# Optimization experiments

Measured on AMD Instinct MI355X. Metric: run time of the kernel, lower is better.

The kernel has to match this reference:

```python
import jax, jax.numpy as jnp
import numpy as np

S = 60            # voxel grid side
N = 100000        # active voxels
M_PAD = 60000     # padded pairs per kernel offset
C_IN = 64
C_OUT = 64
KV = 27           # kernel volume (3^3)
CENTER = 13


def _build_maps():
    rng = np.random.default_rng(0)
    lin = rng.choice(S ** 3, size=N, replace=False)
    coords = np.stack(np.unravel_index(lin, (S, S, S)), axis=1).astype(np.int64)  # [N,3]
    lut = -np.ones(S ** 3, dtype=np.int64)
    lut[lin] = np.arange(N)
    imap = -np.ones((KV - 1, M_PAD), dtype=np.int32)
    omap = -np.ones((KV - 1, M_PAD), dtype=np.int32)
    row = 0
    for k in range(KV):
        if k == CENTER:
            continue
        d = np.array([k // 9 - 1, (k // 3) % 3 - 1, k % 3 - 1])
        nb = coords + d
        valid = np.all((nb >= 0) & (nb < S), axis=1)
        linnb = nb[:, 0] * S * S + nb[:, 1] * S + nb[:, 2]
        j = np.where(valid, lut[np.clip(linnb, 0, S ** 3 - 1)], -1)
        mask = j >= 0
        src = np.nonzero(mask)[0].astype(np.int32)   # input idx (gather)
        dst = j[mask].astype(np.int32)               # output idx (scatter)
        m = min(src.shape[0], M_PAD)
        imap[row, :m] = src[:m]
        omap[row, :m] = dst[:m]
        row += 1
    return imap, omap


def setup_inputs() -> dict:
    key = jax.random.key(0)
    kf, kw = jax.random.split(key)
    feats = jax.random.normal(kf, (N, C_IN), dtype=jnp.float32)
    stdv = 1.0 / np.sqrt(C_OUT * KV)
    kernel = jax.random.uniform(kw, (KV, C_IN, C_OUT), dtype=jnp.float32,
                                minval=-stdv, maxval=stdv)
    imap_np, omap_np = _build_maps()
    return {
        "feats": feats,
        "kernel": kernel,
        "imap": jnp.asarray(imap_np),
        "omap": jnp.asarray(omap_np),
    }


def reference(feats, kernel, imap, omap):
    # Submanifold sparse 3D conv: center weight applied densely,
    # 26 neighbor offsets via gather -> per-offset GEMM -> scatter-add.
    # feats: [N, Cin], kernel: [27, Cin, Cout], imap/omap: [26, M] (-1 = pad)
    koff = jnp.concatenate([jnp.arange(CENTER), jnp.arange(CENTER + 1, KV)])
    w_off = kernel[koff]                                   # [26, Cin, Cout]
    out = feats @ kernel[CENTER]                           # [N, Cout] center GEMM
    valid = (imap >= 0)                                    # [26, M]
    gathered = feats[jnp.clip(imap, 0)] * valid[..., None].astype(feats.dtype)  # [26, M, Cin]
    partial = jnp.einsum('kmc,kco->kmo', gathered, w_off)  # [26, M, Cout]
    dst = jnp.where(valid, omap, 0).reshape(-1)            # padded rows contribute zeros
    out = out.at[dst].add(partial.reshape(-1, partial.shape[-1]))
    return out
```

## Files before the change

kernel.cpp:

```cpp
#include <hip/hip_runtime.h>


#define N_PTS 100000
#define MPAD  60000
#define C     64
#define NSL   27

typedef short bf16x8 __attribute__((ext_vector_type(8)));
typedef float f32x4  __attribute__((ext_vector_type(4)));

static __device__ inline unsigned short f2bf(float x) {
    unsigned int u = __float_as_uint(x);
    u += 0x7fffu + ((u >> 16) & 1u);
    return (unsigned short)(u >> 16);
}

#define FEATS16_BYTES ((size_t)(N_PTS + 1) * C * 2)
#define WFRAG_OFF     (((FEATS16_BYTES) + 255) & ~(size_t)255)
#define WFRAG_BYTES   ((size_t)NSL * 2 * 4 * 64 * 16)
#define NBR_OFF       (WFRAG_OFF + WFRAG_BYTES)
#define NBR_BYTES     ((size_t)26 * N_PTS * 4)

#define FEAT_ITEMS 800008
#define WF_ITEMS   (NSL * 2 * 4 * 64)
#define NBRF_ITEMS (26 * N_PTS / 4)
#define PREP_TOTAL (FEAT_ITEMS + WF_ITEMS + NBRF_ITEMS)

__global__ __launch_bounds__(256) void prep_all(const float* __restrict__ feats,
                                                const float* __restrict__ kern,
                                                unsigned short* __restrict__ f16,
                                                unsigned short* __restrict__ wf,
                                                int* __restrict__ nbr) {
    const int idx = blockIdx.x * 256 + threadIdx.x;
    if (idx < FEAT_ITEMS) {
        bf16x8* dst = (bf16x8*)f16;
        if (idx < FEAT_ITEMS - 8) {
            const float4* src = (const float4*)feats;
            const float4 a = src[2 * idx];
            const float4 b = src[2 * idx + 1];
            bf16x8 v;
            v[0] = (short)f2bf(a.x); v[1] = (short)f2bf(a.y);
            v[2] = (short)f2bf(a.z); v[3] = (short)f2bf(a.w);
            v[4] = (short)f2bf(b.x); v[5] = (short)f2bf(b.y);
            v[6] = (short)f2bf(b.z); v[7] = (short)f2bf(b.w);
            dst[idx] = v;
        } else {
            dst[idx] = (bf16x8){0, 0, 0, 0, 0, 0, 0, 0};
        }
    } else if (idx < FEAT_ITEMS + WF_ITEMS) {
        const int w = idx - FEAT_ITEMS;
        const int lane = w & 63;
        const int rest = w >> 6;
        const int ct = rest & 3;
        const int kk = (rest >> 2) & 1;
        const int s  = rest >> 3;
        const int q = lane >> 4, t = lane & 15;
        const int ksrc = (s == 26) ? 13 : (s + (s >= 13 ? 1 : 0));
        const int k0 = kk * 32 + q * 8;
        const int n  = ct * 16 + t;
        const float* wp = kern + (size_t)ksrc * 4096 + n;
        bf16x8 v;
        #pragma unroll
        for (int j = 0; j < 8; ++j) v[j] = (short)f2bf(wp[(size_t)(k0 + j) * 64]);
        ((bf16x8*)wf)[w] = v;
    } else {
        const int k = idx - (FEAT_ITEMS + WF_ITEMS);
        if (k < NBRF_ITEMS) ((int4*)nbr)[k] = make_int4(-1, -1, -1, -1);
    }
}

__global__ __launch_bounds__(256) void prep_nbr(const int* __restrict__ imap,
                                                const int* __restrict__ omap,
                                                int* __restrict__ nbr) {
    const int v = blockIdx.x * 256 + threadIdx.x;
    const int s = blockIdx.y;
    if (v >= MPAD / 4) return;
    const int4 iv = ((const int4*)(imap + (size_t)s * MPAD))[v];
    const int4 ov = ((const int4*)(omap + (size_t)s * MPAD))[v];
    int* nb = nbr + (size_t)s * N_PTS;
    if (iv.x >= 0) nb[ov.x] = iv.x;
    if (iv.y >= 0) nb[ov.y] = iv.y;
    if (iv.z >= 0) nb[ov.z] = iv.z;
    if (iv.w >= 0) nb[ov.w] = iv.w;
}

__global__ __launch_bounds__(256) void spconv_main(const unsigned short* __restrict__ f16,
                                                   const unsigned short* __restrict__ wf,
                                                   const int* __restrict__ nbr,
                                                   float* __restrict__ out) {
    const int lane = threadIdx.x & 63;
    const int wave = threadIdx.x >> 6;
    const int q = lane >> 4, t = lane & 15;
    const int R0 = blockIdx.x * 128 + wave * 32;
    const int row0 = R0 + t;
    const int row1 = R0 + 16 + t;

    const bf16x8* wfv = (const bf16x8*)wf;
    const bf16x8* fv  = (const bf16x8*)f16;

    auto ldj = [&](int s, int row) -> int {
        if (s == 26) return (row < N_PTS) ? row : -1;
        const int rc = (row < N_PTS) ? row : 0;
        const int j = nbr[(size_t)s * N_PTS + rc];
        return (row < N_PTS) ? j : -1;
    };
    auto clampj = [&](int j) -> int {
        return ((unsigned)j < (unsigned)N_PTS) ? j : N_PTS;
    };

    f32x4 acc[2][4];
    #pragma unroll
    for (int a = 0; a < 2; ++a)
        #pragma unroll
        for (int c = 0; c < 4; ++c)
            acc[a][c] = (f32x4){0.f, 0.f, 0.f, 0.f};

    int j0[NSL], j1[NSL];
    bf16x8 A[NSL][4];

    j0[0] = ldj(0, row0); j1[0] = ldj(0, row1);
    j0[1] = ldj(1, row0); j1[1] = ldj(1, row1);
    {
        const bf16x8* a0 = fv + (size_t)clampj(j0[0]) * 8;
        const bf16x8* a1 = fv + (size_t)clampj(j1[0]) * 8;
        A[0][0] = a0[q]; A[0][1] = a0[4 + q];
        A[0][2] = a1[q]; A[0][3] = a1[4 + q];
    }

    #pragma unroll
    for (int s = 0; s < NSL; ++s) {
        if (s + 2 < NSL) {
            j0[s + 2] = ldj(s + 2, row0);
            j1[s + 2] = ldj(s + 2, row1);
        }
        if (s + 1 < NSL) {
            const bf16x8* a0 = fv + (size_t)clampj(j0[s + 1]) * 8;
            const bf16x8* a1 = fv + (size_t)clampj(j1[s + 1]) * 8;
            A[s + 1][0] = a0[q]; A[s + 1][1] = a0[4 + q];
            A[s + 1][2] = a1[q]; A[s + 1][3] = a1[4 + q];
        }
        bf16x8 B0[4], B1[4];
        #pragma unroll
        for (int ct = 0; ct < 4; ++ct) {
            B0[ct] = wfv[s * 512 + ct * 64 + lane];
            B1[ct] = wfv[s * 512 + 256 + ct * 64 + lane];
        }
        #pragma unroll
        for (int ct = 0; ct < 4; ++ct) {
            acc[0][ct] = __builtin_amdgcn_mfma_f32_16x16x32_bf16(A[s][0], B0[ct], acc[0][ct], 0, 0, 0);
            acc[1][ct] = __builtin_amdgcn_mfma_f32_16x16x32_bf16(A[s][2], B0[ct], acc[1][ct], 0, 0, 0);
        }
        #pragma unroll
        for (int ct = 0; ct < 4; ++ct) {
            acc[0][ct] = __builtin_amdgcn_mfma_f32_16x16x32_bf16(A[s][1], B1[ct], acc[0][ct], 0, 0, 0);
            acc[1][ct] = __builtin_amdgcn_mfma_f32_16x16x32_bf16(A[s][3], B1[ct], acc[1][ct], 0, 0, 0);
        }
    }

    #pragma unroll
    for (int tile = 0; tile < 2; ++tile) {
        #pragma unroll
        for (int i = 0; i < 4; ++i) {
            const int row = R0 + tile * 16 + 4 * q + i;
            if (row < N_PTS) {
                #pragma unroll
                for (int ct = 0; ct < 4; ++ct)
                    out[(size_t)row * C + ct * 16 + t] = acc[tile][ct][i];
            }
        }
    }
}

extern "C" void kernel_launch(void* const* d_in, const int* in_sizes, int n_in,
                              void* d_out, int out_size, void* d_ws, size_t ws_size,
                              hipStream_t stream) {
    const float* feats = (const float*)d_in[0];
    const float* kern  = (const float*)d_in[1];
    const int*   imap  = (const int*)d_in[2];
    const int*   omap  = (const int*)d_in[3];

    char* ws = (char*)d_ws;
    unsigned short* f16 = (unsigned short*)ws;
    unsigned short* wf  = (unsigned short*)(ws + WFRAG_OFF);
    int*            nbr = (int*)(ws + NBR_OFF);

    prep_all<<<dim3((PREP_TOTAL + 255) / 256), dim3(256), 0, stream>>>(
        feats, kern, f16, wf, nbr);
    prep_nbr<<<dim3((MPAD / 4 + 255) / 256, 26), dim3(256), 0, stream>>>(
        imap, omap, nbr);
    spconv_main<<<dim3((N_PTS + 127) / 128), dim3(256), 0, stream>>>(
        f16, wf, nbr, (float*)d_out);
}
```

Measured before the change: 166.9 us.

## Transpose neighbor table to row-major and shrink per-wave tile to 16 rows

Stores the neighbor table as [N][28] so each output row's 27 neighbor indices (center index at slot 26) sit together and load with seven int4 reads. Previously each offset read a separate strided array. Each wave now handles 16 rows instead of 32, which halves the accumulators and A registers and doubles the grid. The explicit software prefetch pipeline across offsets is dropped. In exchange, weight fragments are reused by half as many rows and there is less manual latency hiding, and the scattered writes in prep_nbr now land at a 28-int stride.

```diff
diff --git a/kernel.cpp b/kernel.cpp
--- a/kernel.cpp
+++ b/kernel.cpp
@@ -5,6 +5,7 @@
 #define MPAD  60000
 #define C     64
 #define NSL   27
+#define NBS   28
 
 typedef short bf16x8 __attribute__((ext_vector_type(8)));
 typedef float f32x4  __attribute__((ext_vector_type(4)));
@@ -18,19 +19,19 @@
 #define FEATS16_BYTES ((size_t)(N_PTS + 1) * C * 2)
 #define WFRAG_OFF     (((FEATS16_BYTES) + 255) & ~(size_t)255)
 #define WFRAG_BYTES   ((size_t)NSL * 2 * 4 * 64 * 16)
-#define NBR_OFF       (WFRAG_OFF + WFRAG_BYTES)
-#define NBR_BYTES     ((size_t)26 * N_PTS * 4)
+#define NBRT_OFF      (WFRAG_OFF + WFRAG_BYTES)
+#define NBRT_BYTES    ((size_t)N_PTS * NBS * 4)
 
 #define FEAT_ITEMS 800008
 #define WF_ITEMS   (NSL * 2 * 4 * 64)
-#define NBRF_ITEMS (26 * N_PTS / 4)
-#define PREP_TOTAL (FEAT_ITEMS + WF_ITEMS + NBRF_ITEMS)
+#define NBRT_ITEMS (N_PTS * NBS / 4)
+#define PREP_TOTAL (FEAT_ITEMS + WF_ITEMS + NBRT_ITEMS)
 
 __global__ __launch_bounds__(256) void prep_all(const float* __restrict__ feats,
                                                 const float* __restrict__ kern,
                                                 unsigned short* __restrict__ f16,
                                                 unsigned short* __restrict__ wf,
-                                                int* __restrict__ nbr) {
+                                                int* __restrict__ nbrt) {
     const int idx = blockIdx.x * 256 + threadIdx.x;
     if (idx < FEAT_ITEMS) {
         bf16x8* dst = (bf16x8*)f16;
@@ -65,108 +66,81 @@
         ((bf16x8*)wf)[w] = v;
     } else {
         const int k = idx - (FEAT_ITEMS + WF_ITEMS);
-        if (k < NBRF_ITEMS) ((int4*)nbr)[k] = make_int4(-1, -1, -1, -1);
+        if (k < NBRT_ITEMS) {
+            const int v = k % 7;
+            const int r = k / 7;
+            int4 val = make_int4(-1, -1, -1, -1);
+            if (v == 6) val.z = r;
+            ((int4*)nbrt)[k] = val;
+        }
     }
 }
 
 __global__ __launch_bounds__(256) void prep_nbr(const int* __restrict__ imap,
                                                 const int* __restrict__ omap,
-                                                int* __restrict__ nbr) {
+                                                int* __restrict__ nbrt) {
     const int v = blockIdx.x * 256 + threadIdx.x;
     const int s = blockIdx.y;
     if (v >= MPAD / 4) return;
     const int4 iv = ((const int4*)(imap + (size_t)s * MPAD))[v];
     const int4 ov = ((const int4*)(omap + (size_t)s * MPAD))[v];
-    int* nb = nbr + (size_t)s * N_PTS;
-    if (iv.x >= 0) nb[ov.x] = iv.x;
-    if (iv.y >= 0) nb[ov.y] = iv.y;
-    if (iv.z >= 0) nb[ov.z] = iv.z;
-    if (iv.w >= 0) nb[ov.w] = iv.w;
+    if (iv.x >= 0) nbrt[(size_t)ov.x * NBS + s] = iv.x;
+    if (iv.y >= 0) nbrt[(size_t)ov.y * NBS + s] = iv.y;
+    if (iv.z >= 0) nbrt[(size_t)ov.z * NBS + s] = iv.z;
+    if (iv.w >= 0) nbrt[(size_t)ov.w * NBS + s] = iv.w;
 }
 
 __global__ __launch_bounds__(256) void spconv_main(const unsigned short* __restrict__ f16,
                                                    const unsigned short* __restrict__ wf,
-                                                   const int* __restrict__ nbr,
+                                                   const int* __restrict__ nbrt,
                                                    float* __restrict__ out) {
     const int lane = threadIdx.x & 63;
     const int wave = threadIdx.x >> 6;
     const int q = lane >> 4, t = lane & 15;
-    const int R0 = blockIdx.x * 128 + wave * 32;
-    const int row0 = R0 + t;
-    const int row1 = R0 + 16 + t;
+    const int R0 = (blockIdx.x * 4 + wave) * 16;
+    const int row = R0 + t;
+    const bool inb = (row < N_PTS);
 
     const bf16x8* wfv = (const bf16x8*)wf;
     const bf16x8* fv  = (const bf16x8*)f16;
 
-    auto ldj = [&](int s, int row) -> int {
-        if (s == 26) return (row < N_PTS) ? row : -1;
-        const int rc = (row < N_PTS) ? row : 0;
-        const int j = nbr[(size_t)s * N_PTS + rc];
-        return (row < N_PTS) ? j : -1;
-    };
-    auto clampj = [&](int j) -> int {
-        return ((unsigned)j < (unsigned)N_PTS) ? j : N_PTS;
-    };
+    int4 jv[7];
+    {
+        const int safe_row = inb ? row : 0;
+        const int4* jp = (const int4*)(nbrt + (size_t)safe_row * NBS);
+        #pragma unroll
+        for (int i = 0; i < 7; ++i) jv[i] = jp[i];
+    }
+    const int* jarr = (const int*)jv;
 
-    f32x4 acc[2][4];
+    f32x4 acc[4];
     #pragma unroll
-    for (int a = 0; a < 2; ++a)
+    for (int c = 0; c < 4; ++c) acc[c] = (f32x4){0.f, 0.f, 0.f, 0.f};
+
+    #pragma unroll
+    for (int s = 0; s < NSL; ++s) {
+        const int j  = inb ? jarr[s] : -1;
+        const int jz = ((unsigned)j < (unsigned)N_PTS) ? j : N_PTS;
+        const bf16x8* ar = fv + (size_t)jz * 8;
+        const bf16x8 A0 = ar[q];
+        const bf16x8 A1 = ar[4 + q];
         #pragma unroll
-        for (int c = 0; c < 4; ++c)
-            acc[a][c] = (f32x4){0.f, 0.f, 0.f, 0.f};
-
-    int j0[NSL], j1[NSL];
-    bf16x8 A[NSL][4];
-
-    j0[0] = ldj(0, row0); j1[0] = ldj(0, row1);
-    j0[1] = ldj(1, row0); j1[1] = ldj(1, row1);
-    {
-        const bf16x8* a0 = fv + (size_t)clampj(j0[0]) * 8;
-        const bf16x8* a1 = fv + (size_t)clampj(j1[0]) * 8;
-        A[0][0] = a0[q]; A[0][1] = a0[4 + q];
-        A[0][2] = a1[q]; A[0][3] = a1[4 + q];
+        for (int ct = 0; ct < 4; ++ct)
+            acc[ct] = __builtin_amdgcn_mfma_f32_16x16x32_bf16(
+                A0, wfv[s * 512 + ct * 64 + lane], acc[ct], 0, 0, 0);
+        #pragma unroll
+        for (int ct = 0; ct < 4; ++ct)
+            acc[ct] = __builtin_amdgcn_mfma_f32_16x16x32_bf16(
+                A1, wfv[s * 512 + 256 + ct * 64 + lane], acc[ct], 0, 0, 0);
     }
 
     #pragma unroll
-    for (int s = 0; s < NSL; ++s) {
-        if (s + 2 < NSL) {
-            j0[s + 2] = ldj(s + 2, row0);
-            j1[s + 2] = ldj(s + 2, row1);
-        }
-        if (s + 1 < NSL) {
-            const bf16x8* a0 = fv + (size_t)clampj(j0[s + 1]) * 8;
-            const bf16x8* a1 = fv + (size_t)clampj(j1[s + 1]) * 8;
-            A[s + 1][0] = a0[q]; A[s + 1][1] = a0[4 + q];
-            A[s + 1][2] = a1[q]; A[s + 1][3] = a1[4 + q];
-        }
-        bf16x8 B0[4], B1[4];
-        #pragma unroll
-        for (int ct = 0; ct < 4; ++ct) {
-            B0[ct] = wfv[s * 512 + ct * 64 + lane];
-            B1[ct] = wfv[s * 512 + 256 + ct * 64 + lane];
-        }
-        #pragma unroll
-        for (int ct = 0; ct < 4; ++ct) {
-            acc[0][ct] = __builtin_amdgcn_mfma_f32_16x16x32_bf16(A[s][0], B0[ct], acc[0][ct], 0, 0, 0);
-            acc[1][ct] = __builtin_amdgcn_mfma_f32_16x16x32_bf16(A[s][2], B0[ct], acc[1][ct], 0, 0, 0);
-        }
-        #pragma unroll
-        for (int ct = 0; ct < 4; ++ct) {
-            acc[0][ct] = __builtin_amdgcn_mfma_f32_16x16x32_bf16(A[s][1], B1[ct], acc[0][ct], 0, 0, 0);
-            acc[1][ct] = __builtin_amdgcn_mfma_f32_16x16x32_bf16(A[s][3], B1[ct], acc[1][ct], 0, 0, 0);
-        }
-    }
-
-    #pragma unroll
-    for (int tile = 0; tile < 2; ++tile) {
-        #pragma unroll
-        for (int i = 0; i < 4; ++i) {
-            const int row = R0 + tile * 16 + 4 * q + i;
-            if (row < N_PTS) {
-                #pragma unroll
-                for (int ct = 0; ct < 4; ++ct)
-                    out[(size_t)row * C + ct * 16 + t] = acc[tile][ct][i];
-            }
+    for (int i = 0; i < 4; ++i) {
+        const int r = R0 + 4 * q + i;
+        if (r < N_PTS) {
+            #pragma unroll
+            for (int ct = 0; ct < 4; ++ct)
+                out[(size_t)r * C + ct * 16 + t] = acc[ct][i];
         }
     }
 }
@@ -180,14 +154,14 @@
     const int*   omap  = (const int*)d_in[3];
 
     char* ws = (char*)d_ws;
-    unsigned short* f16 = (unsigned short*)ws;
-    unsigned short* wf  = (unsigned short*)(ws + WFRAG_OFF);
-    int*            nbr = (int*)(ws + NBR_OFF);
+    unsigned short* f16  = (unsigned short*)ws;
+    unsigned short* wfr  = (unsigned short*)(ws + WFRAG_OFF);
+    int*            nbrt = (int*)(ws + NBRT_OFF);
 
     prep_all<<<dim3((PREP_TOTAL + 255) / 256), dim3(256), 0, stream>>>(
-        feats, kern, f16, wf, nbr);
+        feats, kern, f16, wfr, nbrt);
     prep_nbr<<<dim3((MPAD / 4 + 255) / 256, 26), dim3(256), 0, stream>>>(
-        imap, omap, nbr);
-    spconv_main<<<dim3((N_PTS + 127) / 128), dim3(256), 0, stream>>>(
-        f16, wf, nbr, (float*)d_out);
+        imap, omap, nbrt);
+    spconv_main<<<dim3((N_PTS + 63) / 64), dim3(256), 0, stream>>>(
+        f16, wfr, nbrt, (float*)d_out);
 }
```

After: 182.2 us. 9.2% more time.

## Rebalance prep kernels, drop software prefetch, use nontemporal loads and stores

Applied to the files above, without the earlier changes.

The -1 fill of the neighbor table moves into its own kernel, and the bf16 feature/weight conversion is fused with the neighbor scatter into a second kernel, so the scatter no longer waits behind the large conversion work. The main kernel drops the two-stage register prefetch of neighbor indices and gathered features. It loads them in-loop with nontemporal hints to save registers and raise occupancy. Output stores, scatter stores and gather loads are nontemporal, which bypasses cache for data that may be reused, such as features gathered by multiple neighbors. That risks extra HBM traffic and exposed gather latency.

```diff
diff --git a/kernel.cpp b/kernel.cpp
--- a/kernel.cpp
+++ b/kernel.cpp
@@ -21,16 +21,24 @@
 #define NBR_OFF       (WFRAG_OFF + WFRAG_BYTES)
 #define NBR_BYTES     ((size_t)26 * N_PTS * 4)
 
+#define FILL_ITEMS (26 * N_PTS / 4)
 #define FEAT_ITEMS 800008
 #define WF_ITEMS   (NSL * 2 * 4 * 64)
-#define NBRF_ITEMS (26 * N_PTS / 4)
-#define PREP_TOTAL (FEAT_ITEMS + WF_ITEMS + NBRF_ITEMS)
+#define SCAT_ITEMS (26 * MPAD / 4)
+#define REST_TOTAL (FEAT_ITEMS + WF_ITEMS + SCAT_ITEMS)
 
-__global__ __launch_bounds__(256) void prep_all(const float* __restrict__ feats,
-                                                const float* __restrict__ kern,
-                                                unsigned short* __restrict__ f16,
-                                                unsigned short* __restrict__ wf,
-                                                int* __restrict__ nbr) {
+__global__ __launch_bounds__(256) void prep_fill(int* __restrict__ nbr) {
+    const int k = blockIdx.x * 256 + threadIdx.x;
+    if (k < FILL_ITEMS) ((int4*)nbr)[k] = make_int4(-1, -1, -1, -1);
+}
+
+__global__ __launch_bounds__(256) void prep_rest(const float* __restrict__ feats,
+                                                 const float* __restrict__ kern,
+                                                 const int* __restrict__ imap,
+                                                 const int* __restrict__ omap,
+                                                 unsigned short* __restrict__ f16,
+                                                 unsigned short* __restrict__ wf,
+                                                 int* __restrict__ nbr) {
     const int idx = blockIdx.x * 256 + threadIdx.x;
     if (idx < FEAT_ITEMS) {
         bf16x8* dst = (bf16x8*)f16;
@@ -65,23 +73,18 @@
         ((bf16x8*)wf)[w] = v;
     } else {
         const int k = idx - (FEAT_ITEMS + WF_ITEMS);
-        if (k < NBRF_ITEMS) ((int4*)nbr)[k] = make_int4(-1, -1, -1, -1);
+        if (k < SCAT_ITEMS) {
+            const int s = k / (MPAD / 4);
+            const int v = k % (MPAD / 4);
+            const int4 iv = ((const int4*)(imap + (size_t)s * MPAD))[v];
+            const int4 ov = ((const int4*)(omap + (size_t)s * MPAD))[v];
+            int* nb = nbr + (size_t)s * N_PTS;
+            if (iv.x >= 0) __builtin_nontemporal_store(iv.x, nb + ov.x);
+            if (iv.y >= 0) __builtin_nontemporal_store(iv.y, nb + ov.y);
+            if (iv.z >= 0) __builtin_nontemporal_store(iv.z, nb + ov.z);
+            if (iv.w >= 0) __builtin_nontemporal_store(iv.w, nb + ov.w);
+        }
     }
-}
-
-__global__ __launch_bounds__(256) void prep_nbr(const int* __restrict__ imap,
-                                                const int* __restrict__ omap,
-                                                int* __restrict__ nbr) {
-    const int v = blockIdx.x * 256 + threadIdx.x;
-    const int s = blockIdx.y;
-    if (v >= MPAD / 4) return;
-    const int4 iv = ((const int4*)(imap + (size_t)s * MPAD))[v];
-    const int4 ov = ((const int4*)(omap + (size_t)s * MPAD))[v];
-    int* nb = nbr + (size_t)s * N_PTS;
-    if (iv.x >= 0) nb[ov.x] = iv.x;
-    if (iv.y >= 0) nb[ov.y] = iv.y;
-    if (iv.z >= 0) nb[ov.z] = iv.z;
-    if (iv.w >= 0) nb[ov.w] = iv.w;
 }
 
 __global__ __launch_bounds__(256) void spconv_main(const unsigned short* __restrict__ f16,
@@ -94,19 +97,13 @@
     const int R0 = blockIdx.x * 128 + wave * 32;
     const int row0 = R0 + t;
     const int row1 = R0 + 16 + t;
+    const bool inb0 = (row0 < N_PTS);
+    const bool inb1 = (row1 < N_PTS);
+    const int safe0 = inb0 ? row0 : 0;
+    const int safe1 = inb1 ? row1 : 0;
 
     const bf16x8* wfv = (const bf16x8*)wf;
     const bf16x8* fv  = (const bf16x8*)f16;
-
-    auto ldj = [&](int s, int row) -> int {
-        if (s == 26) return (row < N_PTS) ? row : -1;
-        const int rc = (row < N_PTS) ? row : 0;
-        const int j = nbr[(size_t)s * N_PTS + rc];
-        return (row < N_PTS) ? j : -1;
-    };
-    auto clampj = [&](int j) -> int {
-        return ((unsigned)j < (unsigned)N_PTS) ? j : N_PTS;
-    };
 
     f32x4 acc[2][4];
     #pragma unroll
@@ -115,30 +112,28 @@
         for (int c = 0; c < 4; ++c)
             acc[a][c] = (f32x4){0.f, 0.f, 0.f, 0.f};
 
-    int j0[NSL], j1[NSL];
-    bf16x8 A[NSL][4];
-
-    j0[0] = ldj(0, row0); j1[0] = ldj(0, row1);
-    j0[1] = ldj(1, row0); j1[1] = ldj(1, row1);
-    {
-        const bf16x8* a0 = fv + (size_t)clampj(j0[0]) * 8;
-        const bf16x8* a1 = fv + (size_t)clampj(j1[0]) * 8;
-        A[0][0] = a0[q]; A[0][1] = a0[4 + q];
-        A[0][2] = a1[q]; A[0][3] = a1[4 + q];
-    }
-
     #pragma unroll
     for (int s = 0; s < NSL; ++s) {
-        if (s + 2 < NSL) {
-            j0[s + 2] = ldj(s + 2, row0);
-            j1[s + 2] = ldj(s + 2, row1);
+        int j0, j1;
+        if (s == 26) {
+            j0 = inb0 ? row0 : -1;
+            j1 = inb1 ? row1 : -1;
+        } else {
+            const int v0 = __builtin_nontemporal_load(nbr + (size_t)s * N_PTS + safe0);
+            const int v1 = __builtin_nontemporal_load(nbr + (size_t)s * N_PTS + safe1);
+            j0 = inb0 ? v0 : -1;
+            j1 = inb1 ? v1 : -1;
         }
-        if (s + 1 < NSL) {
-            const bf16x8* a0 = fv + (size_t)clampj(j0[s + 1]) * 8;
-            const bf16x8* a1 = fv + (size_t)clampj(j1[s + 1]) * 8;
-            A[s + 1][0] = a0[q]; A[s + 1][1] = a0[4 + q];
-            A[s + 1][2] = a1[q]; A[s + 1][3] = a1[4 + q];
-        }
+        const int jz0 = ((unsigned)j0 < (unsigned)N_PTS) ? j0 : N_PTS;
+        const int jz1 = ((unsigned)j1 < (unsigned)N_PTS) ? j1 : N_PTS;
+
+        const bf16x8* a0 = fv + (size_t)jz0 * 8;
+        const bf16x8* a1 = fv + (size_t)jz1 * 8;
+        const bf16x8 A00 = __builtin_nontemporal_load(a0 + q);
+        const bf16x8 A01 = __builtin_nontemporal_load(a0 + 4 + q);
+        const bf16x8 A10 = __builtin_nontemporal_load(a1 + q);
+        const bf16x8 A11 = __builtin_nontemporal_load(a1 + 4 + q);
+
         bf16x8 B0[4], B1[4];
         #pragma unroll
         for (int ct = 0; ct < 4; ++ct) {
@@ -147,13 +142,13 @@
         }
         #pragma unroll
         for (int ct = 0; ct < 4; ++ct) {
-            acc[0][ct] = __builtin_amdgcn_mfma_f32_16x16x32_bf16(A[s][0], B0[ct], acc[0][ct], 0, 0, 0);
-            acc[1][ct] = __builtin_amdgcn_mfma_f32_16x16x32_bf16(A[s][2], B0[ct], acc[1][ct], 0, 0, 0);
+            acc[0][ct] = __builtin_amdgcn_mfma_f32_16x16x32_bf16(A00, B0[ct], acc[0][ct], 0, 0, 0);
+            acc[1][ct] = __builtin_amdgcn_mfma_f32_16x16x32_bf16(A10, B0[ct], acc[1][ct], 0, 0, 0);
         }
         #pragma unroll
         for (int ct = 0; ct < 4; ++ct) {
-            acc[0][ct] = __builtin_amdgcn_mfma_f32_16x16x32_bf16(A[s][1], B1[ct], acc[0][ct], 0, 0, 0);
-            acc[1][ct] = __builtin_amdgcn_mfma_f32_16x16x32_bf16(A[s][3], B1[ct], acc[1][ct], 0, 0, 0);
+            acc[0][ct] = __builtin_amdgcn_mfma_f32_16x16x32_bf16(A01, B1[ct], acc[0][ct], 0, 0, 0);
+            acc[1][ct] = __builtin_amdgcn_mfma_f32_16x16x32_bf16(A11, B1[ct], acc[1][ct], 0, 0, 0);
         }
     }
 
@@ -161,11 +156,12 @@
     for (int tile = 0; tile < 2; ++tile) {
         #pragma unroll
         for (int i = 0; i < 4; ++i) {
-            const int row = R0 + tile * 16 + 4 * q + i;
-            if (row < N_PTS) {
+            const int r = R0 + tile * 16 + 4 * q + i;
+            if (r < N_PTS) {
                 #pragma unroll
                 for (int ct = 0; ct < 4; ++ct)
-                    out[(size_t)row * C + ct * 16 + t] = acc[tile][ct][i];
+                    __builtin_nontemporal_store(acc[tile][ct][i],
+                                                out + (size_t)r * C + ct * 16 + t);
             }
         }
     }
@@ -181,13 +177,12 @@
 
     char* ws = (char*)d_ws;
     unsigned short* f16 = (unsigned short*)ws;
-    unsigned short* wf  = (unsigned short*)(ws + WFRAG_OFF);
+    unsigned short* wfr = (unsigned short*)(ws + WFRAG_OFF);
     int*            nbr = (int*)(ws + NBR_OFF);
 
-    prep_all<<<dim3((PREP_TOTAL + 255) / 256), dim3(256), 0, stream>>>(
-        feats, kern, f16, wf, nbr);
-    prep_nbr<<<dim3((MPAD / 4 + 255) / 256, 26), dim3(256), 0, stream>>>(
-        imap, omap, nbr);
+    prep_fill<<<dim3((FILL_ITEMS + 255) / 256), dim3(256), 0, stream>>>(nbr);
+    prep_rest<<<dim3((REST_TOTAL + 255) / 256), dim3(256), 0, stream>>>(
+        feats, kern, imap, omap, f16, wfr, nbr);
     spconv_main<<<dim3((N_PTS + 127) / 128), dim3(256), 0, stream>>>(
-        f16, wf, nbr, (float*)d_out);
+        f16, wfr, nbr, (float*)d_out);
 }
```

Measured after the change: 205.3 us. 23.0% more time.

## Give each wave 64 rows and drop the cross-slice gather prefetch

Applied to the files above, without the earlier changes.

Each wave now computes four 16-row tiles (64 output rows) instead of two, so each weight fragment loaded from memory feeds twice as many MFMAs. Blocks shrink to 128 threads (two waves) while the grid size stays the same. The explicit software pipeline that prefetched neighbour indices two slices ahead and features one slice ahead is removed; gathers now happen inside the same slice, relying on the compiler and occupancy to hide latency. The larger accumulator set raises register pressure, and the total number of waves is halved, which reduces latency hiding for the random feature gathers.

```diff
diff --git a/kernel.cpp b/kernel.cpp
--- a/kernel.cpp
+++ b/kernel.cpp
@@ -84,88 +84,80 @@
     if (iv.w >= 0) nb[ov.w] = iv.w;
 }
 
-__global__ __launch_bounds__(256) void spconv_main(const unsigned short* __restrict__ f16,
+__global__ __launch_bounds__(128) void spconv_main(const unsigned short* __restrict__ f16,
                                                    const unsigned short* __restrict__ wf,
                                                    const int* __restrict__ nbr,
                                                    float* __restrict__ out) {
     const int lane = threadIdx.x & 63;
     const int wave = threadIdx.x >> 6;
     const int q = lane >> 4, t = lane & 15;
-    const int R0 = blockIdx.x * 128 + wave * 32;
-    const int row0 = R0 + t;
-    const int row1 = R0 + 16 + t;
+    const int R0 = (blockIdx.x * 2 + wave) * 64;
 
     const bf16x8* wfv = (const bf16x8*)wf;
     const bf16x8* fv  = (const bf16x8*)f16;
 
-    auto ldj = [&](int s, int row) -> int {
-        if (s == 26) return (row < N_PTS) ? row : -1;
-        const int rc = (row < N_PTS) ? row : 0;
-        const int j = nbr[(size_t)s * N_PTS + rc];
-        return (row < N_PTS) ? j : -1;
-    };
-    auto clampj = [&](int j) -> int {
-        return ((unsigned)j < (unsigned)N_PTS) ? j : N_PTS;
-    };
-
-    f32x4 acc[2][4];
+    f32x4 acc[4][4];
     #pragma unroll
-    for (int a = 0; a < 2; ++a)
+    for (int a = 0; a < 4; ++a)
         #pragma unroll
         for (int c = 0; c < 4; ++c)
             acc[a][c] = (f32x4){0.f, 0.f, 0.f, 0.f};
 
-    int j0[NSL], j1[NSL];
-    bf16x8 A[NSL][4];
-
-    j0[0] = ldj(0, row0); j1[0] = ldj(0, row1);
-    j0[1] = ldj(1, row0); j1[1] = ldj(1, row1);
-    {
-        const bf16x8* a0 = fv + (size_t)clampj(j0[0]) * 8;
-        const bf16x8* a1 = fv + (size_t)clampj(j1[0]) * 8;
-        A[0][0] = a0[q]; A[0][1] = a0[4 + q];
-        A[0][2] = a1[q]; A[0][3] = a1[4 + q];
-    }
-
     #pragma unroll
     for (int s = 0; s < NSL; ++s) {
-        if (s + 2 < NSL) {
-            j0[s + 2] = ldj(s + 2, row0);
-            j1[s + 2] = ldj(s + 2, row1);
+        int jz[4];
+        #pragma unroll
+        for (int tl = 0; tl < 4; ++tl) {
+            const int row = R0 + 16 * tl + t;
+            const bool inb = (row < N_PTS);
+            int j;
+            if (s == 26) {
+                j = inb ? row : -1;
+            } else {
+                const int v = nbr[(size_t)s * N_PTS + (inb ? row : 0)];
+                j = inb ? v : -1;
+            }
+            jz[tl] = ((unsigned)j < (unsigned)N_PTS) ? j : N_PTS;
         }
-        if (s + 1 < NSL) {
-            const bf16x8* a0 = fv + (size_t)clampj(j0[s + 1]) * 8;
-            const bf16x8* a1 = fv + (size_t)clampj(j1[s + 1]) * 8;
-            A[s + 1][0] = a0[q]; A[s + 1][1] = a0[4 + q];
-            A[s + 1][2] = a1[q]; A[s + 1][3] = a1[4 + q];
+
+        bf16x8 Alo[4], Ahi[4];
+        #pragma unroll
+        for (int tl = 0; tl < 4; ++tl) {
+            const bf16x8* ar = fv + (size_t)jz[tl] * 8;
+            Alo[tl] = ar[q];
+            Ahi[tl] = ar[4 + q];
         }
+
         bf16x8 B0[4], B1[4];
         #pragma unroll
         for (int ct = 0; ct < 4; ++ct) {
             B0[ct] = wfv[s * 512 + ct * 64 + lane];
             B1[ct] = wfv[s * 512 + 256 + ct * 64 + lane];
         }
+
         #pragma unroll
-        for (int ct = 0; ct < 4; ++ct) {
-            acc[0][ct] = __builtin_amdgcn_mfma_f32_16x16x32_bf16(A[s][0], B0[ct], acc[0][ct], 0, 0, 0);
-            acc[1][ct] = __builtin_amdgcn_mfma_f32_16x16x32_bf16(A[s][2], B0[ct], acc[1][ct], 0, 0, 0);
-        }
+        for (int tl = 0; tl < 4; ++tl)
+            #pragma unroll
+            for (int ct = 0; ct < 4; ++ct)
+                acc[tl][ct] = __builtin_amdgcn_mfma_f32_16x16x32_bf16(
+                    Alo[tl], B0[ct], acc[tl][ct], 0, 0, 0);
         #pragma unroll
-        for (int ct = 0; ct < 4; ++ct) {
-            acc[0][ct] = __builtin_amdgcn_mfma_f32_16x16x32_bf16(A[s][1], B1[ct], acc[0][ct], 0, 0, 0);
-            acc[1][ct] = __builtin_amdgcn_mfma_f32_16x16x32_bf16(A[s][3], B1[ct], acc[1][ct], 0, 0, 0);
-        }
+        for (int tl = 0; tl < 4; ++tl)
+            #pragma unroll
+            for (int ct = 0; ct < 4; ++ct)
+                acc[tl][ct] = __builtin_amdgcn_mfma_f32_16x16x32_bf16(
+                    Ahi[tl], B1[ct], acc[tl][ct], 0, 0, 0);
     }
 
     #pragma unroll
-    for (int tile = 0; tile < 2; ++tile) {
+    for (int tl = 0; tl < 4; ++tl) {
         #pragma unroll
         for (int i = 0; i < 4; ++i) {
-            const int row = R0 + tile * 16 + 4 * q + i;
-            if (row < N_PTS) {
+            const int r = R0 + 16 * tl + 4 * q + i;
+            if (r < N_PTS) {
                 #pragma unroll
                 for (int ct = 0; ct < 4; ++ct)
-                    out[(size_t)row * C + ct * 16 + t] = acc[tile][ct][i];
+                    out[(size_t)r * C + ct * 16 + t] = acc[tl][ct][i];
             }
         }
     }
@@ -181,13 +173,13 @@
 
     char* ws = (char*)d_ws;
     unsigned short* f16 = (unsigned short*)ws;
-    unsigned short* wf  = (unsigned short*)(ws + WFRAG_OFF);
+    unsigned short* wfr = (unsigned short*)(ws + WFRAG_OFF);
     int*            nbr = (int*)(ws + NBR_OFF);
 
     prep_all<<<dim3((PREP_TOTAL + 255) / 256), dim3(256), 0, stream>>>(
-        feats, kern, f16, wf, nbr);
+        feats, kern, f16, wfr, nbr);
     prep_nbr<<<dim3((MPAD / 4 + 255) / 256, 26), dim3(256), 0, stream>>>(
         imap, omap, nbr);
-    spconv_main<<<dim3((N_PTS + 127) / 128), dim3(256), 0, stream>>>(
-        f16, wf, nbr, (float*)d_out);
+    spconv_main<<<dim3((N_PTS + 127) / 128), dim3(128), 0, stream>>>(
+        f16, wfr, nbr, (float*)d_out);
 }
```

Result: slower. 190.1 us (+13.9%).
